# Kernel tuning notes

Measured on AMD Instinct MI355X. Metric: run time of the kernel, lower is better.

The kernel has to match this reference:

```python
import jax, jax.numpy as jnp
import numpy as np

L = 320
C = 128          # pair_embedding_dim
H = 4            # triangle_attention_heads
D = C // H       # head_dim = 32


def setup_inputs() -> dict:
    key = jax.random.key(0)
    ks = jax.random.split(key, 11)
    s = 1.0 / np.sqrt(C)
    inp = {
        "pair_repr": jax.random.normal(ks[0], (L, L, C), dtype=jnp.float32),
        "Wq": jax.random.normal(ks[1], (C, C), dtype=jnp.float32) * s,
        "bq": jnp.zeros((C,), jnp.float32),
        "Wk": jax.random.normal(ks[2], (C, C), dtype=jnp.float32) * s,
        "bk": jnp.zeros((C,), jnp.float32),
        "Wv": jax.random.normal(ks[3], (C, C), dtype=jnp.float32) * s,
        "bv": jnp.zeros((C,), jnp.float32),
        "Wo": jax.random.normal(ks[4], (C, C), dtype=jnp.float32) * s,
        "bo": jnp.zeros((C,), jnp.float32),
        "Wg": jax.random.normal(ks[5], (C, C), dtype=jnp.float32) * s,
        "bg": jnp.zeros((C,), jnp.float32),
    }
    return inp


def reference(pair_repr, Wq, bq, Wk, bk, Wv, bv, Wo, bo, Wg, bg):
    # Triangle attention, 'outgoing' orientation (attention over the second
    # index j of pair_repr[i, :, :], independently for each row i).
    Ldim = pair_repr.shape[0]
    q = (pair_repr @ Wq + bq).reshape(Ldim, Ldim, H, D)
    k = (pair_repr @ Wk + bk).reshape(Ldim, Ldim, H, D)
    v = (pair_repr @ Wv + bv).reshape(Ldim, Ldim, H, D)
    # scores: (L, H, L_q=k-index, L_k=j-index)
    scores = jnp.einsum('ikhd,ijhd->ihkj', q, k) / np.float32(np.sqrt(D))
    attn = jax.nn.softmax(scores, axis=-1)
    out = jnp.einsum('ihkj,ijhd->ikhd', attn, v).reshape(Ldim, Ldim, C)
    out = out @ Wo + bo
    gate = jax.nn.sigmoid(pair_repr @ Wg + bg)
    return out * gate
```

## Files before the change

kernel.cpp:

```cpp
#include <hip/hip_runtime.h>
#include <hip/hip_bf16.h>

#define LL 320
#define CC 128
#define HH 4
#define DD 32
#define MM (LL*LL)

typedef float f32x4 __attribute__((ext_vector_type(4)));
typedef short bf16x8 __attribute__((ext_vector_type(8)));

static __device__ __forceinline__ unsigned short f2b(float f) {
    union { float f; unsigned u; } v; v.f = f;
    unsigned r = (v.u + 0x7fffu + ((v.u >> 16) & 1u)) >> 16;
    return (unsigned short)r;
}
static __device__ __forceinline__ float b2f(unsigned short b) {
    union { unsigned u; float f; } v; v.u = ((unsigned)b) << 16;
    return v.f;
}
static __device__ __forceinline__ unsigned cvtpk(float a, float b) {
    unsigned r;
    asm("v_cvt_pk_bf16_f32 %0, %1, %2" : "=v"(r) : "v"(a), "v"(b));
    return r;
}

__global__ void wtr_kernel(const float* __restrict__ W0, const float* __restrict__ W1,
                           const float* __restrict__ W2, const float* __restrict__ W3,
                           const float* __restrict__ W4, unsigned short* __restrict__ WT)
{
    int mat = blockIdx.y;
    const float* W = (mat == 0) ? W0 : (mat == 1) ? W1 : (mat == 2) ? W2 : (mat == 3) ? W3 : W4;
    unsigned short* dst = WT + (size_t)mat * CC * CC;
    int n0 = blockIdx.x * 8;
    int t = threadIdx.x;
#pragma unroll
    for (int e = 0; e < 4; ++e) {
        int idx = t + e * 256;
        int k = idx & 127, nn = idx >> 7;
        dst[(n0 + nn) * CC + k] = f2b(W[k * CC + n0 + nn]);
    }
}

__launch_bounds__(256)
__global__ void proj_kernel(const float* __restrict__ X, const unsigned short* __restrict__ WT,
                            const float* __restrict__ bq, const float* __restrict__ bk,
                            const float* __restrict__ bv, const float* __restrict__ bg,
                            unsigned short* __restrict__ qb, unsigned short* __restrict__ kb,
                            unsigned short* __restrict__ vb, unsigned short* __restrict__ gb)
{
    __shared__ unsigned char lds[16384 + 32768];
    const int t = threadIdx.x;
    const int m0 = blockIdx.x * 64;

#pragma unroll
    for (int it = 0; it < 8; ++it) {
        int idx = t + it * 256;
        int row = idx >> 5, c4 = idx & 31;
        float4 f = *(const float4*)(X + (size_t)(m0 + row) * CC + c4 * 4);
        unsigned off = (unsigned)(row * 256) + (((unsigned)(c4 * 8)) ^ (((unsigned)(row & 7)) << 4));
        unsigned* p = (unsigned*)(lds + off);
        p[0] = (unsigned)f2b(f.x) | ((unsigned)f2b(f.y) << 16);
        p[1] = (unsigned)f2b(f.z) | ((unsigned)f2b(f.w) << 16);
    }

    const int lane = t & 63, w = t >> 6;
    const int lr = lane & 15, g = lane >> 4;
    const int wr = w >> 1, wc = w & 1;

#pragma unroll
    for (int mat = 0; mat < 4; ++mat) {
        __syncthreads();
        const unsigned short* wsrc = WT + (size_t)mat * CC * CC;
#pragma unroll
        for (int it = 0; it < 8; ++it) {
            int idx = t + it * 256;
            int row = idx >> 4, c = idx & 15;
            uint4 d = *(const uint4*)(wsrc + row * CC + c * 8);
            *(uint4*)(lds + 16384 + row * 256u + (((unsigned)(c * 16)) ^ (((unsigned)(row & 7)) << 4))) = d;
        }
        __syncthreads();

        f32x4 acc[2][4] = {};
#pragma unroll
        for (int kk = 0; kk < 4; ++kk) {
            bf16x8 a[2], b[4];
#pragma unroll
            for (int m = 0; m < 2; ++m) {
                int row = wr * 32 + m * 16 + lr;
                a[m] = *(const bf16x8*)(lds + row * 256u +
                        (((unsigned)(kk * 64 + g * 16)) ^ (((unsigned)(row & 7)) << 4)));
            }
#pragma unroll
            for (int n = 0; n < 4; ++n) {
                int row = wc * 64 + n * 16 + lr;
                b[n] = *(const bf16x8*)(lds + 16384 + row * 256u +
                        (((unsigned)(kk * 64 + g * 16)) ^ (((unsigned)(row & 7)) << 4)));
            }
#pragma unroll
            for (int m = 0; m < 2; ++m)
#pragma unroll
                for (int n = 0; n < 4; ++n)
                    acc[m][n] = __builtin_amdgcn_mfma_f32_16x16x32_bf16(a[m], b[n], acc[m][n], 0, 0, 0);
        }

        const float* bias = (mat == 0) ? bq : (mat == 1) ? bk : (mat == 2) ? bv : bg;
        unsigned short* op = (mat == 0) ? qb : (mat == 1) ? kb : (mat == 2) ? vb : gb;
#pragma unroll
        for (int m = 0; m < 2; ++m)
#pragma unroll
            for (int n = 0; n < 4; ++n) {
                int col = wc * 64 + n * 16 + lr;
                float bs = bias[col];
#pragma unroll
                for (int r = 0; r < 4; ++r) {
                    int row = m0 + wr * 32 + m * 16 + g * 4 + r;
                    float v = acc[m][n][r] + bs;
                    if (mat == 3) v = 1.0f / (1.0f + __expf(-v));
                    op[(size_t)row * CC + col] = f2b(v);
                }
            }
    }
}

__launch_bounds__(256)
__global__ void attn_kernel(const unsigned short* __restrict__ qb, const unsigned short* __restrict__ kb,
                            const unsigned short* __restrict__ vb, unsigned short* __restrict__ ab)
{
    __shared__ unsigned char lds[20480 + 20480];
    const int i = blockIdx.x, h = blockIdx.y;
    const int t = threadIdx.x;
    const size_t base = ((size_t)i * LL) * CC + h * DD;

#pragma unroll
    for (int it = 0; it < 5; ++it) {
        int idx = t + it * 256;
        int j = idx >> 2, ch = idx & 3;
        uint4 d = *(const uint4*)(kb + base + (size_t)j * CC + ch * 8);
        *(uint4*)(lds + j * 64u + ((unsigned)(ch ^ (j & 3)) << 4)) = d;
    }
#pragma unroll
    for (int it = 0; it < 5; ++it) {
        int idx = t + it * 256;
        int j = idx >> 2, ch = idx & 3;
        uint4 d = *(const uint4*)(vb + base + (size_t)j * CC + ch * 8);
        const unsigned short* ev = (const unsigned short*)&d;
#pragma unroll
        for (int u = 0; u < 8; ++u) {
            int dd = ch * 8 + u;
            unsigned off = 20480u + dd * 640u + (((unsigned)((j >> 3) ^ (dd & 7))) << 4) + (j & 7) * 2;
            *(unsigned short*)(lds + off) = ev[u];
        }
    }

    const int lane = t & 63, w = t >> 6;
    const int lr = lane & 15, g = lane >> 4;

    bf16x8 qf[5];
#pragma unroll
    for (int f = 0; f < 5; ++f) {
        int q = w * 80 + f * 16 + lr;
        qf[f] = *(const bf16x8*)(qb + base + (size_t)q * CC + g * 8);
    }
    __syncthreads();

    f32x4 acc[5][2] = {};
    float lsum[5] = {};
    const float sc = 0.25506601f;
    f32x4 zero = {0.f, 0.f, 0.f, 0.f};

    for (int c = 0; c < 10; ++c) {
        bf16x8 kf[2];
#pragma unroll
        for (int tt = 0; tt < 2; ++tt) {
            int j = c * 32 + tt * 16 + lr;
            kf[tt] = *(const bf16x8*)(lds + j * 64u + ((unsigned)(g ^ (j & 3)) << 4));
        }
        union { bf16x8 v; uint2 u2[2]; } vfrag[2];
#pragma unroll
        for (int df = 0; df < 2; ++df) {
            int dd = df * 16 + lr;
            unsigned rowb = 20480u + dd * 640u + (unsigned)(g & 1) * 8;
            unsigned s0 = (unsigned)((c * 4 + (g >> 1)) ^ (dd & 7));
            unsigned s1 = (unsigned)((c * 4 + (g >> 1) + 2) ^ (dd & 7));
            vfrag[df].u2[0] = *(const uint2*)(lds + rowb + (s0 << 4));
            vfrag[df].u2[1] = *(const uint2*)(lds + rowb + (s1 << 4));
        }
#pragma unroll
        for (int f = 0; f < 5; ++f) {
            f32x4 s0 = __builtin_amdgcn_mfma_f32_16x16x32_bf16(kf[0], qf[f], zero, 0, 0, 0);
            f32x4 s1 = __builtin_amdgcn_mfma_f32_16x16x32_bf16(kf[1], qf[f], zero, 0, 0, 0);
            float p0 = __builtin_amdgcn_exp2f(s0[0] * sc), p1 = __builtin_amdgcn_exp2f(s0[1] * sc);
            float p2 = __builtin_amdgcn_exp2f(s0[2] * sc), p3 = __builtin_amdgcn_exp2f(s0[3] * sc);
            float p4 = __builtin_amdgcn_exp2f(s1[0] * sc), p5 = __builtin_amdgcn_exp2f(s1[1] * sc);
            float p6 = __builtin_amdgcn_exp2f(s1[2] * sc), p7 = __builtin_amdgcn_exp2f(s1[3] * sc);
            lsum[f] += ((p0 + p1) + (p2 + p3)) + ((p4 + p5) + (p6 + p7));
            union { bf16x8 v; unsigned u[4]; } pf;
            pf.u[0] = cvtpk(p0, p1);
            pf.u[1] = cvtpk(p2, p3);
            pf.u[2] = cvtpk(p4, p5);
            pf.u[3] = cvtpk(p6, p7);
            acc[f][0] = __builtin_amdgcn_mfma_f32_16x16x32_bf16(vfrag[0].v, pf.v, acc[f][0], 0, 0, 0);
            acc[f][1] = __builtin_amdgcn_mfma_f32_16x16x32_bf16(vfrag[1].v, pf.v, acc[f][1], 0, 0, 0);
        }
    }

#pragma unroll
    for (int f = 0; f < 5; ++f) {
        float l = lsum[f];
        l += __shfl_xor(l, 16);
        l += __shfl_xor(l, 32);
        float inv = 1.0f / l;
        int q = w * 80 + f * 16 + lr;
        size_t orow = base + (size_t)q * CC;
#pragma unroll
        for (int df = 0; df < 2; ++df) {
            uint2 ov = {cvtpk(acc[f][df][0] * inv, acc[f][df][1] * inv),
                        cvtpk(acc[f][df][2] * inv, acc[f][df][3] * inv)};
            *(uint2*)(ab + orow + df * 16 + g * 4) = ov;
        }
    }
}

__launch_bounds__(256)
__global__ void out_kernel(const unsigned short* __restrict__ ab, const unsigned short* __restrict__ WT,
                           const float* __restrict__ bo, const unsigned short* __restrict__ gb,
                           float* __restrict__ out)
{
    __shared__ unsigned char lds[16384 + 32768];
    const int t = threadIdx.x;
    const int m0 = blockIdx.x * 64;
#pragma unroll
    for (int it = 0; it < 4; ++it) {
        int idx = t + it * 256;
        int row = idx >> 4, c = idx & 15;
        uint4 d = *(const uint4*)(ab + (size_t)(m0 + row) * CC + c * 8);
        *(uint4*)(lds + row * 256u + (((unsigned)(c * 16)) ^ (((unsigned)(row & 7)) << 4))) = d;
    }
    const unsigned short* wsrc = WT + (size_t)4 * CC * CC;
#pragma unroll
    for (int it = 0; it < 8; ++it) {
        int idx = t + it * 256;
        int row = idx >> 4, c = idx & 15;
        uint4 d = *(const uint4*)(wsrc + row * CC + c * 8);
        *(uint4*)(lds + 16384 + row * 256u + (((unsigned)(c * 16)) ^ (((unsigned)(row & 7)) << 4))) = d;
    }
    __syncthreads();

    const int lane = t & 63, w = t >> 6;
    const int lr = lane & 15, g = lane >> 4;
    const int wr = w >> 1, wc = w & 1;
    f32x4 acc[2][4] = {};
#pragma unroll
    for (int kk = 0; kk < 4; ++kk) {
        bf16x8 a[2], b[4];
#pragma unroll
        for (int m = 0; m < 2; ++m) {
            int row = wr * 32 + m * 16 + lr;
            a[m] = *(const bf16x8*)(lds + row * 256u +
                    (((unsigned)(kk * 64 + g * 16)) ^ (((unsigned)(row & 7)) << 4)));
        }
#pragma unroll
        for (int n = 0; n < 4; ++n) {
            int row = wc * 64 + n * 16 + lr;
            b[n] = *(const bf16x8*)(lds + 16384 + row * 256u +
                    (((unsigned)(kk * 64 + g * 16)) ^ (((unsigned)(row & 7)) << 4)));
        }
#pragma unroll
        for (int m = 0; m < 2; ++m)
#pragma unroll
            for (int n = 0; n < 4; ++n)
                acc[m][n] = __builtin_amdgcn_mfma_f32_16x16x32_bf16(a[m], b[n], acc[m][n], 0, 0, 0);
    }
#pragma unroll
    for (int m = 0; m < 2; ++m)
#pragma unroll
        for (int n = 0; n < 4; ++n) {
            int col = wc * 64 + n * 16 + lr;
            float bs = bo[col];
#pragma unroll
            for (int r = 0; r < 4; ++r) {
                int row = m0 + wr * 32 + m * 16 + g * 4 + r;
                float y = acc[m][n][r] + bs;
                float gt = b2f(gb[(size_t)row * CC + col]);
                out[(size_t)row * CC + col] = y * gt;
            }
        }
}

extern "C" void kernel_launch(void* const* d_in, const int* in_sizes, int n_in,
                              void* d_out, int out_size, void* d_ws, size_t ws_size,
                              hipStream_t stream)
{
    const float* pair = (const float*)d_in[0];
    const float* Wq = (const float*)d_in[1];  const float* bq = (const float*)d_in[2];
    const float* Wk = (const float*)d_in[3];  const float* bk = (const float*)d_in[4];
    const float* Wv = (const float*)d_in[5];  const float* bv = (const float*)d_in[6];
    const float* Wo = (const float*)d_in[7];  const float* bo = (const float*)d_in[8];
    const float* Wg = (const float*)d_in[9];  const float* bg = (const float*)d_in[10];

    char* ws = (char*)d_ws;
    unsigned short* WT = (unsigned short*)ws;
    const size_t MAT = (size_t)MM * CC * 2;
    unsigned short* qb   = (unsigned short*)(ws + 262144);
    unsigned short* kb   = (unsigned short*)(ws + 262144 + 1 * MAT);
    unsigned short* vb   = (unsigned short*)(ws + 262144 + 2 * MAT);
    unsigned short* gb   = (unsigned short*)(ws + 262144 + 3 * MAT);
    unsigned short* abuf = qb;

    hipLaunchKernelGGL(wtr_kernel, dim3(16, 5), dim3(256), 0, stream, Wq, Wk, Wv, Wg, Wo, WT);
    hipLaunchKernelGGL(proj_kernel, dim3(MM / 64), dim3(256), 0, stream,
                       pair, WT, bq, bk, bv, bg, qb, kb, vb, gb);
    hipLaunchKernelGGL(attn_kernel, dim3(LL, HH), dim3(256), 0, stream, qb, kb, vb, abuf);
    hipLaunchKernelGGL(out_kernel, dim3(MM / 64), dim3(256), 0, stream, abuf, WT, bo, gb, (float*)d_out);
}
```

Measured before the change: 196.7 us.

## Load MFMA operands directly from global memory, dropping LDS staging in projection kernels

The projection and output GEMM kernels no longer stage the activation tile and weight matrix through shared memory. Each wave now loads its MFMA fragments straight from global memory: X rows are converted to bf16 in registers once and reused across all four weight matrices, and weight fragments are read from global (L2-resident) on every use. This removes the LDS writes, the swizzle arithmetic and the __syncthreads barriers, and frees LDS so more blocks can be resident. In exchange the weight matrix is fetched redundantly by every wave, relying on cache hits, and the per-lane loads are less coalesced.

```diff
diff --git a/kernel.cpp b/kernel.cpp
--- a/kernel.cpp
+++ b/kernel.cpp
@@ -49,59 +49,47 @@
                             unsigned short* __restrict__ qb, unsigned short* __restrict__ kb,
                             unsigned short* __restrict__ vb, unsigned short* __restrict__ gb)
 {
-    __shared__ unsigned char lds[16384 + 32768];
     const int t = threadIdx.x;
     const int m0 = blockIdx.x * 64;
-
-#pragma unroll
-    for (int it = 0; it < 8; ++it) {
-        int idx = t + it * 256;
-        int row = idx >> 5, c4 = idx & 31;
-        float4 f = *(const float4*)(X + (size_t)(m0 + row) * CC + c4 * 4);
-        unsigned off = (unsigned)(row * 256) + (((unsigned)(c4 * 8)) ^ (((unsigned)(row & 7)) << 4));
-        unsigned* p = (unsigned*)(lds + off);
-        p[0] = (unsigned)f2b(f.x) | ((unsigned)f2b(f.y) << 16);
-        p[1] = (unsigned)f2b(f.z) | ((unsigned)f2b(f.w) << 16);
-    }
-
     const int lane = t & 63, w = t >> 6;
     const int lr = lane & 15, g = lane >> 4;
     const int wr = w >> 1, wc = w & 1;
 
+    bf16x8 af[2][4];
+#pragma unroll
+    for (int m = 0; m < 2; ++m) {
+        int row = m0 + wr * 32 + m * 16 + lr;
+        const float* xp = X + (size_t)row * CC + g * 8;
+#pragma unroll
+        for (int kk = 0; kk < 4; ++kk) {
+            float4 f0 = *(const float4*)(xp + kk * 32);
+            float4 f1 = *(const float4*)(xp + kk * 32 + 4);
+            union { bf16x8 v; unsigned u[4]; } a;
+            a.u[0] = cvtpk(f0.x, f0.y);
+            a.u[1] = cvtpk(f0.z, f0.w);
+            a.u[2] = cvtpk(f1.x, f1.y);
+            a.u[3] = cvtpk(f1.z, f1.w);
+            af[m][kk] = a.v;
+        }
+    }
+
 #pragma unroll
     for (int mat = 0; mat < 4; ++mat) {
-        __syncthreads();
         const unsigned short* wsrc = WT + (size_t)mat * CC * CC;
-#pragma unroll
-        for (int it = 0; it < 8; ++it) {
-            int idx = t + it * 256;
-            int row = idx >> 4, c = idx & 15;
-            uint4 d = *(const uint4*)(wsrc + row * CC + c * 8);
-            *(uint4*)(lds + 16384 + row * 256u + (((unsigned)(c * 16)) ^ (((unsigned)(row & 7)) << 4))) = d;
-        }
-        __syncthreads();
-
         f32x4 acc[2][4] = {};
 #pragma unroll
         for (int kk = 0; kk < 4; ++kk) {
-            bf16x8 a[2], b[4];
-#pragma unroll
-            for (int m = 0; m < 2; ++m) {
-                int row = wr * 32 + m * 16 + lr;
-                a[m] = *(const bf16x8*)(lds + row * 256u +
-                        (((unsigned)(kk * 64 + g * 16)) ^ (((unsigned)(row & 7)) << 4)));
-            }
+            bf16x8 b[4];
 #pragma unroll
             for (int n = 0; n < 4; ++n) {
                 int row = wc * 64 + n * 16 + lr;
-                b[n] = *(const bf16x8*)(lds + 16384 + row * 256u +
-                        (((unsigned)(kk * 64 + g * 16)) ^ (((unsigned)(row & 7)) << 4)));
+                b[n] = *(const bf16x8*)(wsrc + row * CC + kk * 32 + g * 8);
             }
 #pragma unroll
             for (int m = 0; m < 2; ++m)
 #pragma unroll
                 for (int n = 0; n < 4; ++n)
-                    acc[m][n] = __builtin_amdgcn_mfma_f32_16x16x32_bf16(a[m], b[n], acc[m][n], 0, 0, 0);
+                    acc[m][n] = __builtin_amdgcn_mfma_f32_16x16x32_bf16(af[m][kk], b[n], acc[m][n], 0, 0, 0);
         }
 
         const float* bias = (mat == 0) ? bq : (mat == 1) ? bk : (mat == 2) ? bv : bg;
@@ -227,44 +215,26 @@
                            const float* __restrict__ bo, const unsigned short* __restrict__ gb,
                            float* __restrict__ out)
 {
-    __shared__ unsigned char lds[16384 + 32768];
     const int t = threadIdx.x;
     const int m0 = blockIdx.x * 64;
-#pragma unroll
-    for (int it = 0; it < 4; ++it) {
-        int idx = t + it * 256;
-        int row = idx >> 4, c = idx & 15;
-        uint4 d = *(const uint4*)(ab + (size_t)(m0 + row) * CC + c * 8);
-        *(uint4*)(lds + row * 256u + (((unsigned)(c * 16)) ^ (((unsigned)(row & 7)) << 4))) = d;
-    }
-    const unsigned short* wsrc = WT + (size_t)4 * CC * CC;
-#pragma unroll
-    for (int it = 0; it < 8; ++it) {
-        int idx = t + it * 256;
-        int row = idx >> 4, c = idx & 15;
-        uint4 d = *(const uint4*)(wsrc + row * CC + c * 8);
-        *(uint4*)(lds + 16384 + row * 256u + (((unsigned)(c * 16)) ^ (((unsigned)(row & 7)) << 4))) = d;
-    }
-    __syncthreads();
-
     const int lane = t & 63, w = t >> 6;
     const int lr = lane & 15, g = lane >> 4;
     const int wr = w >> 1, wc = w & 1;
+    const unsigned short* wsrc = WT + (size_t)4 * CC * CC;
+
     f32x4 acc[2][4] = {};
 #pragma unroll
     for (int kk = 0; kk < 4; ++kk) {
         bf16x8 a[2], b[4];
 #pragma unroll
         for (int m = 0; m < 2; ++m) {
-            int row = wr * 32 + m * 16 + lr;
-            a[m] = *(const bf16x8*)(lds + row * 256u +
-                    (((unsigned)(kk * 64 + g * 16)) ^ (((unsigned)(row & 7)) << 4)));
+            int row = m0 + wr * 32 + m * 16 + lr;
+            a[m] = *(const bf16x8*)(ab + (size_t)row * CC + kk * 32 + g * 8);
         }
 #pragma unroll
         for (int n = 0; n < 4; ++n) {
             int row = wc * 64 + n * 16 + lr;
-            b[n] = *(const bf16x8*)(lds + 16384 + row * 256u +
-                    (((unsigned)(kk * 64 + g * 16)) ^ (((unsigned)(row & 7)) << 4)));
+            b[n] = *(const bf16x8*)(wsrc + row * CC + kk * 32 + g * 8);
         }
 #pragma unroll
         for (int m = 0; m < 2; ++m)
```

New measurement: 254.4 us. 29.3% more time.
